# Kernel optimization log

Hardware: AMD Instinct MI355X
Metric: run time of the kernel (lower is better)

## Reference

```python
import jax, jax.numpy as jnp
import numpy as np

N_NODES = 131072
N_EDGES = 2097152
F_IN = 128
G_NODES = 256  # nodes per graph (equal-size graphs -> ptr = arange(0, N+1, 256))


def _linear(x, W, b):
    return x @ W + b


def _gin_conv(x, src, dst, W1, b1, W2, b2):
    # GINConv with eps=0: MLP(x + sum_{j->i} x_j)
    agg = jax.ops.segment_sum(x[src], dst, num_segments=x.shape[0])
    h = jax.nn.relu(_linear(x + agg, W1, b1))
    return _linear(h, W2, b2)


def _init(key, fan_in, fan_out):
    kw, kb = jax.random.split(key)
    s = 1.0 / np.sqrt(fan_in)
    W = jax.random.uniform(kw, (fan_in, fan_out), jnp.float32, -s, s)
    b = jax.random.uniform(kb, (fan_out,), jnp.float32, -s, s)
    return W, b


def setup_inputs() -> dict:
    key = jax.random.key(0)
    ks = jax.random.split(key, 14)
    x = jax.random.normal(ks[0], (N_NODES, F_IN), jnp.float32)
    edge_index = jax.random.randint(ks[1], (2, N_EDGES), 0, N_NODES, jnp.int64)
    W1a, b1a = _init(ks[2], F_IN, 128)
    W2a, b2a = _init(ks[3], 128, 128)
    W1b, b1b = _init(ks[4], 128, 128)
    W2b, b2b = _init(ks[5], 128, 128)
    Ws1, bs1 = _init(ks[6], 128, 32)
    Ws2, bs2 = _init(ks[7], 32, 32)
    Ws3, bs3 = _init(ks[8], 32, 32)
    Wm1, bm1 = _init(ks[9], 32 * 32, 32)
    Wm2, bm2 = _init(ks[10], 32, 32)
    Wm3, bm3 = _init(ks[11], 32, 2)
    return dict(x=x, edge_index=edge_index,
                W1a=W1a, b1a=b1a, W2a=W2a, b2a=b2a,
                W1b=W1b, b1b=b1b, W2b=W2b, b2b=b2b,
                Ws1=Ws1, bs1=bs1, Ws2=Ws2, bs2=bs2, Ws3=Ws3, bs3=bs3,
                Wm1=Wm1, bm1=bm1, Wm2=Wm2, bm2=bm2, Wm3=Wm3, bm3=bm3,
                nodes_per_graph=G_NODES)


def reference(x, edge_index, W1a, b1a, W2a, b2a, W1b, b1b, W2b, b2b,
              Ws1, bs1, Ws2, bs2, Ws3, bs3,
              Wm1, bm1, Wm2, bm2, Wm3, bm3, nodes_per_graph):
    src, dst = edge_index[0], edge_index[1]
    # two GINConv layers, each followed by outer ReLU (as in forward)
    h = jax.nn.relu(_gin_conv(x, src, dst, W1a, b1a, W2a, b2a))
    h = jax.nn.relu(_gin_conv(h, src, dst, W1b, b1b, W2b, b2b))
    # dropout is identity in eval mode; F.normalize(dim=1) row-wise L2
    hn = h / jnp.maximum(jnp.linalg.norm(h, axis=1, keepdims=True), 1e-12)
    s = jax.nn.relu(_linear(hn, Ws1, bs1))
    s = jax.nn.relu(_linear(s, Ws2, bs2))
    s = jax.nn.relu(_linear(s, Ws3, bs3))  # [N, 32]
    G = x.shape[0] // nodes_per_graph
    sg = s.reshape(G, nodes_per_graph, 32)
    # per-graph second-order pooling: graph.T @ graph, flattened
    HH = jnp.einsum('gnf,gne->gfe', sg, sg).reshape(G, 32 * 32)  # [G, 1024]
    o = jax.nn.relu(_linear(HH, Wm1, bm1))
    o = jax.nn.relu(_linear(o, Wm2, bm2))
    out = jax.nn.relu(_linear(o, Wm3, bm3))  # [G, 2]; output dropout identity in eval
    return (HH, out)
```

## Files before the change

kernel.cpp:

```cpp
#include <hip/hip_runtime.h>
#include <hip/hip_bf16.h>


#define NN 131072
#define NE 2097152
#define NG 512
#define NB 1024
#define BCAP 4096
#define ECH 8192
#define CAP 3072

typedef unsigned short u16;
typedef unsigned int u32;
typedef __attribute__((ext_vector_type(8))) short short8;
typedef __attribute__((ext_vector_type(4))) float f32x4;

__device__ __forceinline__ float bf2f(u16 u) {
    union { u32 i; float f; } x; x.i = ((u32)u) << 16; return x.f;
}
__device__ __forceinline__ u16 f2bf(float f) {
    union { u32 i; float f; } x; x.f = f;
    u32 r = x.i + 0x7fffu + ((x.i >> 16) & 1u);
    return (u16)(r >> 16);
}

__global__ __launch_bounds__(256) void cast_x(const float* __restrict__ xf,
                                              u16* __restrict__ xb) {
    int i = blockIdx.x * 256 + threadIdx.x;
    const float4* src = (const float4*)xf;
    float4 a = src[2 * i], b = src[2 * i + 1];
    uint4 o;
    o.x = (u32)f2bf(a.x) | ((u32)f2bf(a.y) << 16);
    o.y = (u32)f2bf(a.z) | ((u32)f2bf(a.w) << 16);
    o.z = (u32)f2bf(b.x) | ((u32)f2bf(b.y) << 16);
    o.w = (u32)f2bf(b.z) | ((u32)f2bf(b.w) << 16);
    ((uint4*)xb)[i] = o;
}

__global__ __launch_bounds__(256) void init_cursor(int* __restrict__ cursor) {
    int b = blockIdx.x * 256 + threadIdx.x;
    cursor[b] = b * BCAP;
}

__global__ __launch_bounds__(256) void bin_scatter(const int* __restrict__ gsrc,
                                                   const int* __restrict__ gdst,
                                                   int* __restrict__ cursor,
                                                   u32* __restrict__ ebuf) {
    __shared__ int lc[NB];
    __shared__ int rb[NB];
    __shared__ int lb[NB];
    int t = threadIdx.x;
    for (int i = 0; i < 4; ++i) lc[t + i * 256] = 0;
    __syncthreads();
    int base = blockIdx.x * ECH;
    for (int i = 0; i < ECH / 256; ++i) {
        int d = gdst[base + i * 256 + t];
        atomicAdd(&lc[d >> 7], 1);
    }
    __syncthreads();
    for (int i = 0; i < 4; ++i) {
        int b = t + i * 256;
        int c = lc[b];
        rb[b] = c ? atomicAdd(&cursor[b], c) : 0;
        lb[b] = 0;
    }
    __syncthreads();
    for (int i = 0; i < ECH / 256; ++i) {
        int idx = base + i * 256 + t;
        int d = gdst[idx];
        int s = gsrc[idx];
        int b = d >> 7;
        int o = atomicAdd(&lb[b], 1);
        ebuf[rb[b] + o] = ((u32)s << 7) | (u32)(d & 127);
    }
}

__global__ __launch_bounds__(512) void aggregate_bucket(const u16* __restrict__ X,
                                                        const u32* __restrict__ ebuf,
                                                        const int* __restrict__ bcur,
                                                        u16* __restrict__ T) {
    __shared__ int lcnt[128];
    __shared__ int lstart[128];
    __shared__ int lofs[128];
    __shared__ int sorted[CAP];
    int t = threadIdx.x, lane = t & 63, wave = t >> 6;
    int bkt = blockIdx.x;
    const u32* Xu = (const u32*)X;

    float a0[16], a1[16];
#pragma unroll
    for (int i = 0; i < 16; ++i) {
        int row = bkt * 128 + wave * 16 + i;
        u32 v = Xu[(size_t)row * 64 + lane];
        a0[i] = bf2f((u16)v);
        a1[i] = bf2f((u16)(v >> 16));
    }

    int e0 = bkt * BCAP, e1 = bcur[bkt];
    for (int cs = e0; cs < e1; cs += CAP) {
        int n = min(CAP, e1 - cs);
        if (t < 128) lcnt[t] = 0;
        __syncthreads();
        for (int j = t; j < n; j += 512)
            atomicAdd(&lcnt[ebuf[cs + j] & 127], 1);
        __syncthreads();
        if (wave == 0) {
            int c0 = lcnt[2 * lane], c1 = lcnt[2 * lane + 1];
            int s = c0 + c1, e = s;
            for (int o = 1; o < 64; o <<= 1) {
                int u = __shfl_up(e, o, 64);
                if (lane >= o) e += u;
            }
            int excl = e - s;
            lstart[2 * lane] = excl;          lofs[2 * lane] = excl;
            lstart[2 * lane + 1] = excl + c0; lofs[2 * lane + 1] = excl + c0;
        }
        __syncthreads();
        for (int j = t; j < n; j += 512) {
            u32 e = ebuf[cs + j];
            int pos = atomicAdd(&lofs[e & 127], 1);
            sorted[pos] = (int)(e >> 7);
        }
        __syncthreads();
#pragma unroll
        for (int i = 0; i < 16; ++i) {
            int node = wave * 16 + i;
            int p = lstart[node], pe = p + lcnt[node];
            for (; p < pe; p += 8) {
                int s[8]; float m[8];
#pragma unroll
                for (int k = 0; k < 8; ++k) {
                    int q = p + k;
                    s[k] = sorted[q < pe ? q : pe - 1];
                    m[k] = (q < pe) ? 1.f : 0.f;
                }
                u32 w[8];
#pragma unroll
                for (int k = 0; k < 8; ++k) w[k] = Xu[(size_t)s[k] * 64 + lane];
#pragma unroll
                for (int k = 0; k < 8; ++k) {
                    a0[i] = fmaf(m[k], bf2f((u16)w[k]), a0[i]);
                    a1[i] = fmaf(m[k], bf2f((u16)(w[k] >> 16)), a1[i]);
                }
            }
        }
        __syncthreads();
    }

    u32* Tu = (u32*)T;
#pragma unroll
    for (int i = 0; i < 16; ++i) {
        int row = bkt * 128 + wave * 16 + i;
        Tu[(size_t)row * 64 + lane] = (u32)f2bf(a0[i]) | ((u32)f2bf(a1[i]) << 16);
    }
}

__global__ __launch_bounds__(256) void transpose_w(const float* a, const float* b,
                                                   const float* c, const float* d, u16* Wt) {
    const float* w = (blockIdx.x == 0) ? a : (blockIdx.x == 1) ? b : (blockIdx.x == 2) ? c : d;
    u16* o = Wt + blockIdx.x * 16384;
    for (int i = 0; i < 64; ++i) {
        int idx = threadIdx.x + i * 256;
        o[(idx & 127) * 128 + (idx >> 7)] = f2bf(w[idx]);
    }
}

__global__ __launch_bounds__(256) void gemm2_relu(const u16* __restrict__ A,
                                                  const u16* __restrict__ Wt1,
                                                  const u16* __restrict__ Wt2,
                                                  const float* __restrict__ b1,
                                                  const float* __restrict__ b2,
                                                  u16* __restrict__ C) {
    __shared__ u16 As[64][136];
    __shared__ u16 Ws[128][136];
    int tid = threadIdx.x;
    size_t rowBase = (size_t)blockIdx.x * 64;

    uint4 w2r[8];
#pragma unroll
    for (int i = 0; i < 8; ++i) {
        int c = tid + i * 256;
        w2r[i] = *(const uint4*)(Wt2 + (c >> 4) * 128 + ((c & 15) << 3));
    }
    for (int i = 0; i < 4; ++i) {
        int c = tid + i * 256;
        int r = c >> 4, co = (c & 15) << 3;
        *(uint4*)&As[r][co] = *(const uint4*)(A + (rowBase + r) * 128 + co);
    }
    for (int i = 0; i < 8; ++i) {
        int c = tid + i * 256;
        int r = c >> 4, co = (c & 15) << 3;
        *(uint4*)&Ws[r][co] = *(const uint4*)(Wt1 + r * 128 + co);
    }
    __syncthreads();

    int lane = tid & 63, wave = tid >> 6;
    int quad = lane >> 4, l16 = lane & 15;

    f32x4 acc[8];
#pragma unroll
    for (int t = 0; t < 8; ++t) acc[t] = (f32x4){0.f, 0.f, 0.f, 0.f};
#pragma unroll
    for (int c = 0; c < 4; ++c) {
        short8 a = *(const short8*)&As[wave * 16 + l16][c * 32 + quad * 8];
#pragma unroll
        for (int t = 0; t < 8; ++t) {
            short8 b = *(const short8*)&Ws[t * 16 + l16][c * 32 + quad * 8];
            acc[t] = __builtin_amdgcn_mfma_f32_16x16x32_bf16(a, b, acc[t], 0, 0, 0);
        }
    }

#pragma unroll
    for (int t = 0; t < 8; ++t) {
        int col = t * 16 + l16;
        float bv = b1[col];
#pragma unroll
        for (int r = 0; r < 4; ++r)
            As[wave * 16 + quad * 4 + r][col] = f2bf(fmaxf(acc[t][r] + bv, 0.f));
    }
    __syncthreads();

#pragma unroll
    for (int i = 0; i < 8; ++i) {
        int c = tid + i * 256;
        *(uint4*)&Ws[c >> 4][(c & 15) << 3] = w2r[i];
    }
    __syncthreads();

    f32x4 acc2[8];
#pragma unroll
    for (int t = 0; t < 8; ++t) acc2[t] = (f32x4){0.f, 0.f, 0.f, 0.f};
#pragma unroll
    for (int c = 0; c < 4; ++c) {
        short8 a = *(const short8*)&As[wave * 16 + l16][c * 32 + quad * 8];
#pragma unroll
        for (int t = 0; t < 8; ++t) {
            short8 b = *(const short8*)&Ws[t * 16 + l16][c * 32 + quad * 8];
            acc2[t] = __builtin_amdgcn_mfma_f32_16x16x32_bf16(a, b, acc2[t], 0, 0, 0);
        }
    }
#pragma unroll
    for (int t = 0; t < 8; ++t) {
        int col = t * 16 + l16;
        float bv = b2[col];
#pragma unroll
        for (int r = 0; r < 4; ++r) {
            int row = wave * 16 + quad * 4 + r;
            C[(rowBase + row) * 128 + col] = f2bf(fmaxf(acc2[t][r] + bv, 0.f));
        }
    }
}

__global__ __launch_bounds__(256) void norm_mlp(const u16* __restrict__ X,
                                                const float* Ws1, const float* bs1,
                                                const float* Ws2, const float* bs2,
                                                const float* Ws3, const float* bs3,
                                                float* __restrict__ S) {
    __shared__ float W1s[128 * 32];
    __shared__ float W2s[32 * 32];
    __shared__ float W3s[32 * 32];
    __shared__ float b1s[32], b2s[32], b3s[32];
    __shared__ float hbuf[4][128];
    __shared__ float sbuf[4][32];
    int t = threadIdx.x;
    for (int i = 0; i < 16; ++i) W1s[t + i * 256] = Ws1[t + i * 256];
    for (int i = 0; i < 4; ++i) { W2s[t + i * 256] = Ws2[t + i * 256]; W3s[t + i * 256] = Ws3[t + i * 256]; }
    if (t < 32) { b1s[t] = bs1[t]; b2s[t] = bs2[t]; b3s[t] = bs3[t]; }
    __syncthreads();

    int wave = t >> 6, lane = t & 63;
    int j = lane & 31, half = lane >> 5;

    for (int it = 0; it < 8; ++it) {
        int node = blockIdx.x * 32 + wave * 8 + it;
        u32 v = ((const u32*)X)[(size_t)node * 64 + lane];
        float f0 = bf2f((u16)v), f1 = bf2f((u16)(v >> 16));
        float ss = f0 * f0 + f1 * f1;
        for (int o = 1; o < 64; o <<= 1) ss += __shfl_xor(ss, o, 64);
        float inv = 1.0f / fmaxf(sqrtf(ss), 1e-12f);
        hbuf[wave][2 * lane] = f0 * inv;
        hbuf[wave][2 * lane + 1] = f1 * inv;
        __syncthreads();

        float p = 0.f;
        for (int i = 0; i < 64; ++i) { int k = half * 64 + i; p += hbuf[wave][k] * W1s[k * 32 + j]; }
        p += __shfl_xor(p, 32, 64);
        float s1 = fmaxf(p + b1s[j], 0.f);
        if (!half) sbuf[wave][j] = s1;
        __syncthreads();

        p = 0.f;
        for (int i = 0; i < 16; ++i) { int k = half * 16 + i; p += sbuf[wave][k] * W2s[k * 32 + j]; }
        p += __shfl_xor(p, 32, 64);
        float s2 = fmaxf(p + b2s[j], 0.f);
        __syncthreads();
        if (!half) sbuf[wave][j] = s2;
        __syncthreads();

        p = 0.f;
        for (int i = 0; i < 16; ++i) { int k = half * 16 + i; p += sbuf[wave][k] * W3s[k * 32 + j]; }
        p += __shfl_xor(p, 32, 64);
        float s3 = fmaxf(p + b3s[j], 0.f);
        if (!half) S[(size_t)node * 32 + j] = s3;
        __syncthreads();
    }
}

__global__ __launch_bounds__(256) void gram(const float* __restrict__ S,
                                            float* __restrict__ out) {
    __shared__ float Sg[256 * 32];
    int t = threadIdx.x, g = blockIdx.x;
    const float4* src = (const float4*)(S + (size_t)g * 8192);
    float4* dst = (float4*)Sg;
    for (int i = 0; i < 8; ++i) dst[t + i * 256] = src[t + i * 256];
    __syncthreads();

    int f = t >> 3, e0 = (t & 7) << 2;
    float4 a = {0.f, 0.f, 0.f, 0.f};
    for (int n = 0; n < 256; ++n) {
        float sf = Sg[n * 32 + f];
        float4 se = *(const float4*)&Sg[n * 32 + e0];
        a.x += sf * se.x; a.y += sf * se.y; a.z += sf * se.z; a.w += sf * se.w;
    }
    *(float4*)(out + (size_t)g * 1024 + f * 32 + e0) = a;
}

__global__ __launch_bounds__(256) void graph_mlp(const float* __restrict__ HH,
                                                 const float* Wm1, const float* bm1,
                                                 const float* Wm2, const float* bm2,
                                                 const float* Wm3, const float* bm3,
                                                 float* __restrict__ out) {
    __shared__ float hh[1024];
    __shared__ float red[256];
    __shared__ float o1[32];
    __shared__ float o2[32];
    int t = threadIdx.x, g = blockIdx.x;
    ((float4*)hh)[t] = ((const float4*)(HH + (size_t)g * 1024))[t];
    __syncthreads();

    int j = t & 31, part = t >> 5;
    float p = 0.f;
    for (int i = 0; i < 128; ++i) { int k = part * 128 + i; p += hh[k] * Wm1[k * 32 + j]; }
    red[t] = p;
    __syncthreads();
    if (t < 32) {
        float s = 0.f;
        for (int q = 0; q < 8; ++q) s += red[q * 32 + t];
        o1[t] = fmaxf(s + bm1[t], 0.f);
    }
    __syncthreads();
    if (t < 32) {
        float s = 0.f;
        for (int k = 0; k < 32; ++k) s += o1[k] * Wm2[k * 32 + t];
        o2[t] = fmaxf(s + bm2[t], 0.f);
    }
    __syncthreads();
    if (t < 2) {
        float s = 0.f;
        for (int k = 0; k < 32; ++k) s += o2[k] * Wm3[k * 2 + t];
        out[524288 + g * 2 + t] = fmaxf(s + bm3[t], 0.f);
    }
}

extern "C" void kernel_launch(void* const* d_in, const int* in_sizes, int n_in,
                              void* d_out, int out_size, void* d_ws, size_t ws_size,
                              hipStream_t stream) {
    const float* x   = (const float*)d_in[0];
    const int*   ei  = (const int*)d_in[1];
    const float* W1a = (const float*)d_in[2];  const float* b1a = (const float*)d_in[3];
    const float* W2a = (const float*)d_in[4];  const float* b2a = (const float*)d_in[5];
    const float* W1b = (const float*)d_in[6];  const float* b1b = (const float*)d_in[7];
    const float* W2b = (const float*)d_in[8];  const float* b2b = (const float*)d_in[9];
    const float* Ws1 = (const float*)d_in[10]; const float* bs1 = (const float*)d_in[11];
    const float* Ws2 = (const float*)d_in[12]; const float* bs2 = (const float*)d_in[13];
    const float* Ws3 = (const float*)d_in[14]; const float* bs3 = (const float*)d_in[15];
    const float* Wm1 = (const float*)d_in[16]; const float* bm1 = (const float*)d_in[17];
    const float* Wm2 = (const float*)d_in[18]; const float* bm2 = (const float*)d_in[19];
    const float* Wm3 = (const float*)d_in[20]; const float* bm3 = (const float*)d_in[21];
    float* out = (float*)d_out;

    const int* gsrc = ei;
    const int* gdst = ei + NE;

    char* ws = (char*)d_ws;
    size_t off = 0;
    auto alloc = [&](size_t bytes) { size_t r = off; off = (off + bytes + 255) & ~(size_t)255; return r; };
    int*  cursor = (int*)(ws + alloc((size_t)NB * 4));
    u32*  ebuf   = (u32*)(ws + alloc((size_t)NB * BCAP * 4));
    u16*  Wt     = (u16*)(ws + alloc(4 * 16384 * 2));
    u16*  X0     = (u16*)(ws + alloc((size_t)NN * 128 * 2));
    u16*  B1     = (u16*)(ws + alloc((size_t)NN * 128 * 2));
    float* S     = (float*)B1;
    (void)ws_size; (void)n_in; (void)in_sizes; (void)out_size;

    init_cursor<<<NB / 256, 256, 0, stream>>>(cursor);
    bin_scatter<<<NE / ECH, 256, 0, stream>>>(gsrc, gdst, cursor, ebuf);

    cast_x<<<NN * 128 / (256 * 8), 256, 0, stream>>>(x, X0);
    transpose_w<<<4, 256, 0, stream>>>(W1a, W2a, W1b, W2b, Wt);

    aggregate_bucket<<<NB, 512, 0, stream>>>(X0, ebuf, cursor, B1);
    gemm2_relu<<<NN / 64, 256, 0, stream>>>(B1, Wt + 0 * 16384, Wt + 1 * 16384, b1a, b2a, X0);
    aggregate_bucket<<<NB, 512, 0, stream>>>(X0, ebuf, cursor, B1);
    gemm2_relu<<<NN / 64, 256, 0, stream>>>(B1, Wt + 2 * 16384, Wt + 3 * 16384, b1b, b2b, X0);

    norm_mlp<<<NN / 32, 256, 0, stream>>>(X0, Ws1, bs1, Ws2, bs2, Ws3, bs3, S);
    gram<<<NG, 256, 0, stream>>>(S, out);
    graph_mlp<<<NG, 256, 0, stream>>>(out, Wm1, bm1, Wm2, bm2, Wm3, bm3, out);
}
```

Before: 586.0 us.

## Rewrite SOPOOL per-node MLP as tiled bf16 MFMA kernel

Replaces the scalar per-node norm+3-layer MLP kernel, which worked one node at a time with many block-wide barriers, with a kernel that normalizes 64 rows into LDS and runs the three linear layers as bf16 MFMA tiles. A new small transpose kernel converts the SOPOOL weights to transposed bf16 once. This is meant to remove the heavy LDS-bound scalar FMA loops and repeated syncs. It adds bf16 rounding of the normalized activations and the intermediate layers.

```diff
diff --git a/kernel.cpp b/kernel.cpp
--- a/kernel.cpp
+++ b/kernel.cpp
@@ -165,6 +165,22 @@
     }
 }
 
+__global__ __launch_bounds__(256) void transpose_small(const float* Ws1, const float* Ws2,
+                                                       const float* Ws3, u16* Wsm) {
+    int t = threadIdx.x;
+    for (int i = 0; i < 16; ++i) {
+        int idx = t + i * 256;
+        int k = idx >> 5, n = idx & 31;
+        Wsm[n * 128 + k] = f2bf(Ws1[idx]);
+    }
+    for (int i = 0; i < 4; ++i) {
+        int idx = t + i * 256;
+        int k = idx >> 5, n = idx & 31;
+        Wsm[4096 + n * 32 + k] = f2bf(Ws2[idx]);
+        Wsm[5120 + n * 32 + k] = f2bf(Ws3[idx]);
+    }
+}
+
 __global__ __launch_bounds__(256) void gemm2_relu(const u16* __restrict__ A,
                                                   const u16* __restrict__ Wt1,
                                                   const u16* __restrict__ Wt2,
@@ -251,58 +267,108 @@
     }
 }
 
-__global__ __launch_bounds__(256) void norm_mlp(const u16* __restrict__ X,
-                                                const float* Ws1, const float* bs1,
-                                                const float* Ws2, const float* bs2,
-                                                const float* Ws3, const float* bs3,
-                                                float* __restrict__ S) {
-    __shared__ float W1s[128 * 32];
-    __shared__ float W2s[32 * 32];
-    __shared__ float W3s[32 * 32];
-    __shared__ float b1s[32], b2s[32], b3s[32];
-    __shared__ float hbuf[4][128];
-    __shared__ float sbuf[4][32];
-    int t = threadIdx.x;
-    for (int i = 0; i < 16; ++i) W1s[t + i * 256] = Ws1[t + i * 256];
-    for (int i = 0; i < 4; ++i) { W2s[t + i * 256] = Ws2[t + i * 256]; W3s[t + i * 256] = Ws3[t + i * 256]; }
-    if (t < 32) { b1s[t] = bs1[t]; b2s[t] = bs2[t]; b3s[t] = bs3[t]; }
-    __syncthreads();
-
-    int wave = t >> 6, lane = t & 63;
-    int j = lane & 31, half = lane >> 5;
-
-    for (int it = 0; it < 8; ++it) {
-        int node = blockIdx.x * 32 + wave * 8 + it;
-        u32 v = ((const u32*)X)[(size_t)node * 64 + lane];
+__global__ __launch_bounds__(256) void norm_mlp_mfma(const u16* __restrict__ X,
+                                                     const u16* __restrict__ Wsm,
+                                                     const float* __restrict__ bs1,
+                                                     const float* __restrict__ bs2,
+                                                     const float* __restrict__ bs3,
+                                                     float* __restrict__ S) {
+    __shared__ u16 As[64][136];
+    __shared__ u16 W1s[32][136];
+    __shared__ u16 W23s[2][32][40];
+    __shared__ u16 H[64][40];
+    int tid = threadIdx.x, lane = tid & 63, wave = tid >> 6;
+    int quad = lane >> 4, l16 = lane & 15;
+    size_t rowBase = (size_t)blockIdx.x * 64;
+
+#pragma unroll
+    for (int i = 0; i < 2; ++i) {
+        int c = tid + i * 256;
+        int r = c >> 4, co = (c & 15) << 3;
+        *(uint4*)&W1s[r][co] = *(const uint4*)(Wsm + r * 128 + co);
+    }
+    {
+        int which = tid >> 7, cc = tid & 127;
+        int r = cc >> 2, co = (cc & 3) << 3;
+        *(uint4*)&W23s[which][r][co] = *(const uint4*)(Wsm + 4096 + which * 1024 + r * 32 + co);
+    }
+
+    const u32* Xu = (const u32*)X;
+    for (int i = 0; i < 16; ++i) {
+        int row = wave * 16 + i;
+        u32 v = Xu[(rowBase + row) * 64 + lane];
         float f0 = bf2f((u16)v), f1 = bf2f((u16)(v >> 16));
         float ss = f0 * f0 + f1 * f1;
         for (int o = 1; o < 64; o <<= 1) ss += __shfl_xor(ss, o, 64);
         float inv = 1.0f / fmaxf(sqrtf(ss), 1e-12f);
-        hbuf[wave][2 * lane] = f0 * inv;
-        hbuf[wave][2 * lane + 1] = f1 * inv;
-        __syncthreads();
-
-        float p = 0.f;
-        for (int i = 0; i < 64; ++i) { int k = half * 64 + i; p += hbuf[wave][k] * W1s[k * 32 + j]; }
-        p += __shfl_xor(p, 32, 64);
-        float s1 = fmaxf(p + b1s[j], 0.f);
-        if (!half) sbuf[wave][j] = s1;
-        __syncthreads();
-
-        p = 0.f;
-        for (int i = 0; i < 16; ++i) { int k = half * 16 + i; p += sbuf[wave][k] * W2s[k * 32 + j]; }
-        p += __shfl_xor(p, 32, 64);
-        float s2 = fmaxf(p + b2s[j], 0.f);
-        __syncthreads();
-        if (!half) sbuf[wave][j] = s2;
-        __syncthreads();
-
-        p = 0.f;
-        for (int i = 0; i < 16; ++i) { int k = half * 16 + i; p += sbuf[wave][k] * W3s[k * 32 + j]; }
-        p += __shfl_xor(p, 32, 64);
-        float s3 = fmaxf(p + b3s[j], 0.f);
-        if (!half) S[(size_t)node * 32 + j] = s3;
-        __syncthreads();
+        *(u32*)&As[row][2 * lane] = (u32)f2bf(f0 * inv) | ((u32)f2bf(f1 * inv) << 16);
+    }
+    __syncthreads();
+
+    f32x4 acc[2];
+    acc[0] = (f32x4){0.f, 0.f, 0.f, 0.f};
+    acc[1] = (f32x4){0.f, 0.f, 0.f, 0.f};
+#pragma unroll
+    for (int c = 0; c < 4; ++c) {
+        short8 a = *(const short8*)&As[wave * 16 + l16][c * 32 + quad * 8];
+#pragma unroll
+        for (int t = 0; t < 2; ++t) {
+            short8 b = *(const short8*)&W1s[t * 16 + l16][c * 32 + quad * 8];
+            acc[t] = __builtin_amdgcn_mfma_f32_16x16x32_bf16(a, b, acc[t], 0, 0, 0);
+        }
+    }
+#pragma unroll
+    for (int t = 0; t < 2; ++t) {
+        int col = t * 16 + l16;
+        float bv = bs1[col];
+#pragma unroll
+        for (int r = 0; r < 4; ++r)
+            H[wave * 16 + quad * 4 + r][col] = f2bf(fmaxf(acc[t][r] + bv, 0.f));
+    }
+    __syncthreads();
+
+    f32x4 acc2[2];
+    acc2[0] = (f32x4){0.f, 0.f, 0.f, 0.f};
+    acc2[1] = (f32x4){0.f, 0.f, 0.f, 0.f};
+    {
+        short8 a = *(const short8*)&H[wave * 16 + l16][quad * 8];
+#pragma unroll
+        for (int t = 0; t < 2; ++t) {
+            short8 b = *(const short8*)&W23s[0][t * 16 + l16][quad * 8];
+            acc2[t] = __builtin_amdgcn_mfma_f32_16x16x32_bf16(a, b, acc2[t], 0, 0, 0);
+        }
+    }
+    __syncthreads();
+#pragma unroll
+    for (int t = 0; t < 2; ++t) {
+        int col = t * 16 + l16;
+        float bv = bs2[col];
+#pragma unroll
+        for (int r = 0; r < 4; ++r)
+            H[wave * 16 + quad * 4 + r][col] = f2bf(fmaxf(acc2[t][r] + bv, 0.f));
+    }
+    __syncthreads();
+
+    f32x4 acc3[2];
+    acc3[0] = (f32x4){0.f, 0.f, 0.f, 0.f};
+    acc3[1] = (f32x4){0.f, 0.f, 0.f, 0.f};
+    {
+        short8 a = *(const short8*)&H[wave * 16 + l16][quad * 8];
+#pragma unroll
+        for (int t = 0; t < 2; ++t) {
+            short8 b = *(const short8*)&W23s[1][t * 16 + l16][quad * 8];
+            acc3[t] = __builtin_amdgcn_mfma_f32_16x16x32_bf16(a, b, acc3[t], 0, 0, 0);
+        }
+    }
+#pragma unroll
+    for (int t = 0; t < 2; ++t) {
+        int col = t * 16 + l16;
+        float bv = bs3[col];
+#pragma unroll
+        for (int r = 0; r < 4; ++r) {
+            int row = wave * 16 + quad * 4 + r;
+            S[(rowBase + row) * 32 + col] = fmaxf(acc3[t][r] + bv, 0.f);
+        }
     }
 }
 
@@ -388,6 +454,7 @@
     int*  cursor = (int*)(ws + alloc((size_t)NB * 4));
     u32*  ebuf   = (u32*)(ws + alloc((size_t)NB * BCAP * 4));
     u16*  Wt     = (u16*)(ws + alloc(4 * 16384 * 2));
+    u16*  Wsm    = (u16*)(ws + alloc(6144 * 2));
     u16*  X0     = (u16*)(ws + alloc((size_t)NN * 128 * 2));
     u16*  B1     = (u16*)(ws + alloc((size_t)NN * 128 * 2));
     float* S     = (float*)B1;
@@ -398,13 +465,14 @@
 
     cast_x<<<NN * 128 / (256 * 8), 256, 0, stream>>>(x, X0);
     transpose_w<<<4, 256, 0, stream>>>(W1a, W2a, W1b, W2b, Wt);
+    transpose_small<<<1, 256, 0, stream>>>(Ws1, Ws2, Ws3, Wsm);
 
     aggregate_bucket<<<NB, 512, 0, stream>>>(X0, ebuf, cursor, B1);
     gemm2_relu<<<NN / 64, 256, 0, stream>>>(B1, Wt + 0 * 16384, Wt + 1 * 16384, b1a, b2a, X0);
     aggregate_bucket<<<NB, 512, 0, stream>>>(X0, ebuf, cursor, B1);
     gemm2_relu<<<NN / 64, 256, 0, stream>>>(B1, Wt + 2 * 16384, Wt + 3 * 16384, b1b, b2b, X0);
 
-    norm_mlp<<<NN / 32, 256, 0, stream>>>(X0, Ws1, bs1, Ws2, bs2, Ws3, bs3, S);
+    norm_mlp_mfma<<<NN / 64, 256, 0, stream>>>(X0, Wsm, bs1, bs2, bs3, S);
     gram<<<NG, 256, 0, stream>>>(S, out);
     graph_mlp<<<NG, 256, 0, stream>>>(out, Wm1, bm1, Wm2, bm2, Wm3, bm3, out);
 }
```

Result: faster. 502.7 us (-14.2%).
